# Kernel tuning notes

Hardware: AMD Instinct MI355X
Metric: run time of the kernel (lower is better)

Reference implementation:

```python
import jax, jax.numpy as jnp
import numpy as np

NL, D, DI, N, R, K = 32, 256, 512, 16, 16, 4   # layers, d_model, d_inner, d_state, dt_rank, d_conv
V, FF, BATCH, L = 4096, 1024, 32, 256


def _mamba_layer(x, p):
    # x: (B, L, D). One pre-norm Mamba block with residual: x + mamba(LN(x)).
    ln_w, ln_b, in_w, cw, cb, xp_w, dtw, dtb, A_log, Dskip, out_w = p
    mu = x.mean(-1, keepdims=True)
    var = ((x - mu) ** 2).mean(-1, keepdims=True)
    h = (x - mu) / jnp.sqrt(var + 1e-5) * ln_w + ln_b
    xz = jnp.einsum('bld,ed->ble', h, in_w)            # (B, L, 2*DI)
    xm, z = jnp.split(xz, 2, axis=-1)
    seq = xm.shape[1]
    # causal depthwise conv1d, kernel K, then SiLU
    xpad = jnp.pad(xm, ((0, 0), (K - 1, 0), (0, 0)))
    xc = sum(xpad[:, k:k + seq] * cw[:, k] for k in range(K)) + cb
    xc = jax.nn.silu(xc)
    dbc = jnp.einsum('ble,fe->blf', xc, xp_w)          # (B, L, R+2N)
    dt, Bm, Cm = jnp.split(dbc, [R, R + N], axis=-1)
    dt = jax.nn.softplus(jnp.einsum('blr,er->ble', dt, dtw) + dtb)  # (B, L, DI)
    A = -jnp.exp(A_log)                                # (DI, N)

    def step(hs, inp):
        dt_t, B_t, C_t, x_t = inp                      # (B,DI),(B,N),(B,N),(B,DI)
        dA = jnp.exp(dt_t[..., None] * A)              # (B, DI, N)
        hs = hs * dA + (dt_t * x_t)[..., None] * B_t[:, None, :]
        return hs, jnp.einsum('ben,bn->be', hs, C_t)

    h0 = jnp.zeros((xc.shape[0], DI, N), xc.dtype)
    _, ys = jax.lax.scan(step, h0, (dt.swapaxes(0, 1), Bm.swapaxes(0, 1), Cm.swapaxes(0, 1), xc.swapaxes(0, 1)))
    y = ys.swapaxes(0, 1) + xc * Dskip
    y = y * jax.nn.silu(z)
    return x + jnp.einsum('ble,de->bld', y, out_w)


def _stack_forward(x, params):
    return jax.lax.scan(lambda c, p: (jax.checkpoint(_mamba_layer)(c, p), None), x, params)[0]


def setup_inputs() -> dict:
    key = jax.random.key(0)
    ks = jax.random.split(key, 12)
    rn = lambda k, shape, s=0.02: jax.random.normal(k, shape, jnp.float32) * s
    return {
        'token_ids': jax.random.randint(ks[0], (BATCH, L), 0, V),
        'emb': rn(ks[1], (V, D)),
        'ln_w': jnp.ones((NL, D)), 'ln_b': jnp.zeros((NL, D)),
        'in_proj_w': rn(ks[2], (NL, 2 * DI, D)),
        'conv_w': rn(ks[3], (NL, DI, K), 0.1), 'conv_b': jnp.zeros((NL, DI)),
        'x_proj_w': rn(ks[4], (NL, R + 2 * N, DI)),
        'dt_w': rn(ks[5], (NL, DI, R), 0.1),
        'dt_b': jnp.full((NL, DI), float(np.log(np.expm1(0.01))), jnp.float32),
        'A_log': jnp.broadcast_to(jnp.log(jnp.arange(1, N + 1, dtype=jnp.float32)), (NL, DI, N)) + 0.0,
        'Dskip': jnp.ones((NL, DI)),
        'out_proj_w': rn(ks[6], (NL, D, DI)),
        'W1': rn(ks[7], (FF, D)), 'b1': jnp.zeros((FF,)),
        'W2': rn(ks[8], (V, FF)), 'b2': jnp.zeros((V,)),
    }


def reference(token_ids, emb, ln_w, ln_b, in_proj_w, conv_w, conv_b, x_proj_w, dt_w, dt_b, A_log, Dskip, out_proj_w, W1, b1, W2, b2):
    x = emb[token_ids]                                  # (B, L, D)
    params = (ln_w, ln_b, in_proj_w, conv_w, conv_b, x_proj_w, dt_w, dt_b, A_log, Dskip, out_proj_w)
    x = _stack_forward(x, params)                       # 32 stacked Mamba blocks
    h = jax.nn.relu(x @ W1.T + b1)
    return h @ W2.T + b2                                # (B, L, V) logits
```

## Files before the change

### kernel.cpp

```cpp
#include <hip/hip_runtime.h>
#include <hip/hip_bf16.h>
#include <cstdint>
#include <cstddef>


typedef __bf16 v8bf __attribute__((ext_vector_type(8)));
typedef float  v4f  __attribute__((ext_vector_type(4)));

__device__ __forceinline__ void async_copy16(const void* g, void* l) {
  __builtin_amdgcn_global_load_lds((const __attribute__((address_space(1))) void*)g,
                                   (__attribute__((address_space(3))) void*)l, 16, 0, 0);
}

__device__ __forceinline__ float bf(__bf16 v) { return (float)v; }

constexpr size_t OFF_WIN  = 0;
constexpr size_t OFF_WXP  = 16777216;
constexpr size_t OFF_WOUT = 18350080;
constexpr size_t OFF_WW1  = 26738688;
constexpr size_t OFF_WW2  = 27262976;
constexpr size_t OFF_X    = 35651584;
constexpr size_t OFF_H    = 44040192;
constexpr size_t OFF_XZ   = 48234496;
constexpr size_t OFF_DBC  = 65011712;
constexpr size_t OFF_PART = 66584576;
constexpr size_t OFF_SS   = 82313216;
constexpr size_t OFF_A2   = 83296256;

__global__ __launch_bounds__(256)
void f2b_multi(const float* __restrict__ s0, const float* __restrict__ s1,
               const float* __restrict__ s2, const float* __restrict__ s3,
               const float* __restrict__ s4, const float* __restrict__ s5,
               char* __restrict__ ws) {
  size_t i = (size_t)blockIdx.x * 256 + threadIdx.x;
  if (i < 8388608) { ((__bf16*)(ws + OFF_WIN))[i] = (__bf16)s0[i]; return; }
  i -= 8388608;
  if (i < 786432)  { ((__bf16*)(ws + OFF_WXP))[i] = (__bf16)s1[i]; return; }
  i -= 786432;
  if (i < 4194304) { ((__bf16*)(ws + OFF_WOUT))[i] = (__bf16)s2[i]; return; }
  i -= 4194304;
  if (i < 262144)  { ((__bf16*)(ws + OFF_WW1))[i] = (__bf16)s3[i]; return; }
  i -= 262144;
  if (i < 4194304) { ((__bf16*)(ws + OFF_WW2))[i] = (__bf16)s4[i]; return; }
  i -= 4194304;
  ((float*)(ws + OFF_A2))[i] = -1.4426950408889634f * __expf(s5[i]);
}

__global__ __launch_bounds__(256) void f2b_k(const float* __restrict__ X,
                                             __bf16* __restrict__ O) {
  size_t i = (size_t)blockIdx.x * 256 + threadIdx.x;
  O[i] = (__bf16)X[i];
}

__global__ __launch_bounds__(256)
void embed_ln_k(const int* __restrict__ tok, const float* __restrict__ emb,
                const float* __restrict__ w, const float* __restrict__ b,
                float* __restrict__ X, __bf16* __restrict__ H) {
  int row = blockIdx.x;
  int t   = threadIdx.x;
  float v = emb[(size_t)tok[row] * 256 + t];
  X[(size_t)row * 256 + t] = v;
  float s = v, q = v * v;
  #pragma unroll
  for (int o = 32; o > 0; o >>= 1) { s += __shfl_xor(s, o); q += __shfl_xor(q, o); }
  __shared__ float ss[4], qq[4];
  int wv = t >> 6;
  if ((t & 63) == 0) { ss[wv] = s; qq[wv] = q; }
  __syncthreads();
  s = ss[0] + ss[1] + ss[2] + ss[3];
  q = qq[0] + qq[1] + qq[2] + qq[3];
  float mu  = s * (1.f / 256.f);
  float var = q * (1.f / 256.f) - mu * mu;
  float r   = rsqrtf(var + 1e-5f);
  H[(size_t)row * 256 + t] = (__bf16)((v - mu) * r * w[t] + b[t]);
}

template <int EPI>
__global__ __launch_bounds__(256, 2)
void gemm_bt(const __bf16* __restrict__ A, const __bf16* __restrict__ W,
             void* outp, const float* __restrict__ bias, int M, int N, int K) {
  __shared__ __align__(16) __bf16 sA[128 * 32];
  __shared__ __align__(16) __bf16 sB[128 * 32];
  const int tid  = threadIdx.x;
  const int bm0  = blockIdx.y << 7;
  const int bn0  = blockIdx.x << 7;
  const int lane = tid & 63;
  const int wv   = tid >> 6;
  const int wm   = (wv >> 1) << 6;
  const int wn   = (wv & 1) << 6;
  const int lr   = lane & 15;
  const int lk   = lane >> 4;

  v4f acc[4][4] = {};

  const int r0 = tid >> 2;
  const int c0 = (tid & 3) << 3;
  const int wbase = (tid & ~63) << 3;

  const __bf16* gA0 = A + (size_t)(bm0 + r0) * K + c0;
  const __bf16* gA1 = A + (size_t)(bm0 + 64 + r0) * K + c0;
  const __bf16* gB0 = W + (size_t)(bn0 + r0) * K + c0;
  const __bf16* gB1 = W + (size_t)(bn0 + 64 + r0) * K + c0;

  for (int kk = 0; kk < K; kk += 32) {
    async_copy16(gA0 + kk, sA + wbase);
    async_copy16(gA1 + kk, sA + 2048 + wbase);
    async_copy16(gB0 + kk, sB + wbase);
    async_copy16(gB1 + kk, sB + 2048 + wbase);
    __syncthreads();
    v8bf af[4], bfr[4];
    #pragma unroll
    for (int i = 0; i < 4; ++i)
      af[i] = *(const v8bf*)(sA + ((wm + i * 16 + lr) << 5) + (lk << 3));
    #pragma unroll
    for (int j = 0; j < 4; ++j)
      bfr[j] = *(const v8bf*)(sB + ((wn + j * 16 + lr) << 5) + (lk << 3));
    #pragma unroll
    for (int i = 0; i < 4; ++i)
      #pragma unroll
      for (int j = 0; j < 4; ++j)
        acc[i][j] = __builtin_amdgcn_mfma_f32_16x16x32_bf16(af[i], bfr[j], acc[i][j], 0, 0, 0);
    __syncthreads();
  }

  #pragma unroll
  for (int i = 0; i < 4; ++i) {
    #pragma unroll
    for (int j = 0; j < 4; ++j) {
      int gc = bn0 + wn + j * 16 + lr;
      #pragma unroll
      for (int v = 0; v < 4; ++v) {
        int gr = bm0 + wm + i * 16 + (lk << 2) + v;
        float val = acc[i][j][v];
        size_t idx = (size_t)gr * N + gc;
        if (EPI == 0) {
          ((__bf16*)outp)[idx] = (__bf16)val;
        } else if (EPI == 1) {
          val += bias[gc]; val = fmaxf(val, 0.f);
          ((__bf16*)outp)[idx] = (__bf16)val;
        } else {
          ((float*)outp)[idx] = val + bias[gc];
        }
      }
    }
  }
}

__global__ __launch_bounds__(512, 4)
void convscan1_k(const __bf16* __restrict__ XZ,
                 const float* __restrict__ cw, const float* __restrict__ cb,
                 const __bf16* __restrict__ Wxp,
                 const float* __restrict__ dtw, const float* __restrict__ dtb,
                 const float* __restrict__ A2,
                 float* __restrict__ DBC,
                 float* __restrict__ PART, float* __restrict__ SS) {
  __shared__ __align__(16) __bf16 sXC[16 * 512];
  __shared__ __align__(16) float  sDBC[16 * 48];
  const int tid = threadIdx.x;
  const int c   = blockIdx.x >> 5;
  const int b   = blockIdx.x & 31;
  const int bl0 = b * 256 + c * 16;

  {
    const int r  = tid >> 5;
    const int ec = tid & 31;
    #pragma unroll
    for (int j = 0; j < 2; ++j) {
      const int e = (ec << 3) + (j << 8);
      v4f cw4[8];
      #pragma unroll
      for (int jj = 0; jj < 8; ++jj) cw4[jj] = *(const v4f*)(cw + (size_t)(e + jj) * 4);
      float a[8];
      #pragma unroll
      for (int jj = 0; jj < 8; ++jj) a[jj] = cb[e + jj];
      #pragma unroll
      for (int k = 0; k < 4; ++k) {
        if (c > 0 || r + k >= 3) {
          const v8bf xv = *(const v8bf*)(XZ + (size_t)(bl0 + r + k - 3) * 1024 + e);
          #pragma unroll
          for (int jj = 0; jj < 8; ++jj) a[jj] += bf(xv[jj]) * cw4[jj][k];
        }
      }
      v8bf outv;
      #pragma unroll
      for (int jj = 0; jj < 8; ++jj) {
        float s = a[jj] / (1.f + __expf(-a[jj]));
        outv[jj] = (__bf16)s;
      }
      const int cbk = (e >> 3) ^ (r & 7);
      *(v8bf*)(sXC + r * 512 + (cbk << 3)) = outv;
    }
  }
  __syncthreads();

  if (tid < 192) {
    const int w = tid >> 6, lane = tid & 63, lr = lane & 15, lk = lane >> 4;
    v4f acc = {};
    for (int kk = 0; kk < 512; kk += 32) {
      const v8bf bfr = *(const v8bf*)(Wxp + (size_t)(w * 16 + lr) * 512 + kk + (lk << 3));
      const int cbk = (((kk >> 3) + lk) ^ (lr & 7));
      const v8bf af = *(const v8bf*)(sXC + lr * 512 + (cbk << 3));
      acc = __builtin_amdgcn_mfma_f32_16x16x32_bf16(af, bfr, acc, 0, 0, 0);
    }
    const int gc = w * 16 + lr;
    #pragma unroll
    for (int v = 0; v < 4; ++v)
      sDBC[((lk << 2) + v) * 48 + gc] = acc[v];
  }
  __syncthreads();

  if (tid < 192)
    *(v4f*)(DBC + (size_t)bl0 * 48 + tid * 4) = *(const v4f*)(sDBC + tid * 4);

  if (c < 15) {
    const int e = tid;
    v4f a2[4], wd[4];
    #pragma unroll
    for (int q = 0; q < 4; ++q) {
      a2[q] = *(const v4f*)(A2  + (size_t)e * 16 + q * 4);
      wd[q] = *(const v4f*)(dtw + (size_t)e * 16 + q * 4);
    }
    const float bias = dtb[e];
    float part[16];
    #pragma unroll
    for (int n = 0; n < 16; ++n) part[n] = 0.f;
    float S = 0.f;
    for (int tt = 0; tt < 16; ++tt) {
      const v4f* dp = (const v4f*)(sDBC + tt * 48);
      float dtv = bias;
      {
        const v4f d0 = dp[0], d1 = dp[1], d2 = dp[2], d3 = dp[3];
        #pragma unroll
        for (int r = 0; r < 4; ++r)
          dtv += d0[r] * wd[0][r] + d1[r] * wd[1][r] + d2[r] * wd[2][r] + d3[r] * wd[3][r];
      }
      dtv = (dtv > 20.f) ? dtv : log1pf(__expf(dtv));
      const float x = bf(sXC[tt * 512 + (((e >> 3) ^ (tt & 7)) << 3) + (e & 7)]);
      const float dtx = dtv * x;
      S += dtv;
      {
        const v4f bv0 = dp[4], bv1 = dp[5], bv2 = dp[6], bv3 = dp[7];
        #pragma unroll
        for (int v = 0; v < 4; ++v) {
          part[v]      = part[v]      * exp2f(dtv * a2[0][v]) + dtx * bv0[v];
          part[4 + v]  = part[4 + v]  * exp2f(dtv * a2[1][v]) + dtx * bv1[v];
          part[8 + v]  = part[8 + v]  * exp2f(dtv * a2[2][v]) + dtx * bv2[v];
          part[12 + v] = part[12 + v] * exp2f(dtv * a2[3][v]) + dtx * bv3[v];
        }
      }
    }
    const size_t o = (((size_t)c * 32 + b) * 512 + e) * 16;
    #pragma unroll
    for (int rq = 0; rq < 4; ++rq) {
      v4f p;
      #pragma unroll
      for (int v = 0; v < 4; ++v) p[v] = part[rq * 4 + v];
      *(v4f*)(PART + o + rq * 4) = p;
    }
    SS[((size_t)c * 32 + b) * 512 + e] = S;
  }
}

__global__ __launch_bounds__(512, 4)
void scan2out_k(const __bf16* __restrict__ XZ,
                const float* __restrict__ cw, const float* __restrict__ cb,
                const float* __restrict__ DBC,
                const float* __restrict__ dtw, const float* __restrict__ dtb,
                const float* __restrict__ A2, const float* __restrict__ Dskip,
                const float* __restrict__ PART, const float* __restrict__ SS,
                const __bf16* __restrict__ Wout,
                const float* __restrict__ lnw, const float* __restrict__ lnb,
                float* __restrict__ X, __bf16* __restrict__ H) {
  __shared__ __align__(16) __bf16 sY[16 * 520];
  __shared__ __align__(16) __bf16 sB[256 * 32];
  __shared__ float sSum[8][16], sSq[8][16];
  const int tid = threadIdx.x;
  const int c   = blockIdx.x >> 5;
  const int b   = blockIdx.x & 31;
  const int bl0 = b * 256 + c * 16;
  const int e   = tid;

  v4f a2[4], wd[4];
  #pragma unroll
  for (int q = 0; q < 4; ++q) {
    a2[q] = *(const v4f*)(A2  + (size_t)e * 16 + q * 4);
    wd[q] = *(const v4f*)(dtw + (size_t)e * 16 + q * 4);
  }
  const float bias = dtb[e];
  const float Dsk  = Dskip[e];
  const v4f   cwv  = *(const v4f*)(cw + (size_t)e * 4);
  const float cbe  = cb[e];

  float h[16];
  #pragma unroll
  for (int n = 0; n < 16; ++n) h[n] = 0.f;
  for (int cc = 0; cc < c; ++cc) {
    const float S  = SS[((size_t)cc * 32 + b) * 512 + e];
    const size_t o = (((size_t)cc * 32 + b) * 512 + e) * 16;
    #pragma unroll
    for (int rq = 0; rq < 4; ++rq) {
      const v4f p = *(const v4f*)(PART + o + rq * 4);
      #pragma unroll
      for (int v = 0; v < 4; ++v)
        h[rq * 4 + v] = h[rq * 4 + v] * exp2f(a2[rq][v] * S) + p[v];
    }
  }

  float w0 = 0.f, w1 = 0.f, w2 = 0.f;
  if (c > 0) {
    w0 = bf(XZ[(size_t)(bl0 - 3) * 1024 + e]);
    w1 = bf(XZ[(size_t)(bl0 - 2) * 1024 + e]);
    w2 = bf(XZ[(size_t)(bl0 - 1) * 1024 + e]);
  }

  for (int tt = 0; tt < 16; ++tt) {
    const float xt = bf(XZ[(size_t)(bl0 + tt) * 1024 + e]);
    float a = cbe + w0 * cwv[0] + w1 * cwv[1] + w2 * cwv[2] + xt * cwv[3];
    const float x = a / (1.f + __expf(-a));
    w0 = w1; w1 = w2; w2 = xt;
    const v4f* dp = (const v4f*)(DBC + (size_t)(bl0 + tt) * 48);
    float dtv = bias;
    {
      const v4f d0 = dp[0], d1 = dp[1], d2 = dp[2], d3 = dp[3];
      #pragma unroll
      for (int r = 0; r < 4; ++r)
        dtv += d0[r] * wd[0][r] + d1[r] * wd[1][r] + d2[r] * wd[2][r] + d3[r] * wd[3][r];
    }
    dtv = (dtv > 20.f) ? dtv : log1pf(__expf(dtv));
    const float dtx = dtv * x;
    float y = 0.f;
    {
      const v4f bv0 = dp[4], bv1 = dp[5], bv2 = dp[6], bv3 = dp[7];
      const v4f cv0 = dp[8], cv1 = dp[9], cv2 = dp[10], cv3 = dp[11];
      #pragma unroll
      for (int v = 0; v < 4; ++v) {
        h[v]      = h[v]      * exp2f(dtv * a2[0][v]) + dtx * bv0[v];  y += h[v]      * cv0[v];
        h[4 + v]  = h[4 + v]  * exp2f(dtv * a2[1][v]) + dtx * bv1[v];  y += h[4 + v]  * cv1[v];
        h[8 + v]  = h[8 + v]  * exp2f(dtv * a2[2][v]) + dtx * bv2[v];  y += h[8 + v]  * cv2[v];
        h[12 + v] = h[12 + v] * exp2f(dtv * a2[3][v]) + dtx * bv3[v];  y += h[12 + v] * cv3[v];
      }
    }
    const float z  = bf(XZ[(size_t)(bl0 + tt) * 1024 + 512 + e]);
    const float sg = z / (1.f + __expf(-z));
    sY[tt * 520 + e] = (__bf16)((y + x * Dsk) * sg);
  }
  __syncthreads();

  const int w = tid >> 6, lane = tid & 63, lr = lane & 15, lk = lane >> 4;
  const int wn = w << 5;
  v4f acc[2] = {};
  for (int kk = 0; kk < 512; kk += 32) {
    async_copy16(Wout + (size_t)(tid >> 2) * 512 + ((tid & 3) << 3) + kk,
                 sB + ((tid & ~63) << 3));
    async_copy16(Wout + (size_t)(128 + (tid >> 2)) * 512 + ((tid & 3) << 3) + kk,
                 sB + 4096 + ((tid & ~63) << 3));
    __syncthreads();
    const v8bf af = *(const v8bf*)(sY + lr * 520 + kk + (lk << 3));
    #pragma unroll
    for (int j = 0; j < 2; ++j) {
      const v8bf bfr = *(const v8bf*)(sB + ((wn + j * 16 + lr) << 5) + (lk << 3));
      acc[j] = __builtin_amdgcn_mfma_f32_16x16x32_bf16(af, bfr, acc[j], 0, 0, 0);
    }
    __syncthreads();
  }

  float s2[4], q2[4];
  #pragma unroll
  for (int v = 0; v < 4; ++v) {
    const int gr = bl0 + (lk << 2) + v;
    float s = 0.f, q = 0.f;
    #pragma unroll
    for (int j = 0; j < 2; ++j) {
      const int gc = wn + j * 16 + lr;
      float val = X[(size_t)gr * 256 + gc] + acc[j][v];
      acc[j][v] = val;
      s += val; q += val * val;
    }
    #pragma unroll
    for (int o = 8; o > 0; o >>= 1) { s += __shfl_xor(s, o); q += __shfl_xor(q, o); }
    s2[v] = s; q2[v] = q;
  }
  if (lr == 0) {
    #pragma unroll
    for (int v = 0; v < 4; ++v) {
      const int row = (lk << 2) + v;
      sSum[w][row] = s2[v];
      sSq[w][row]  = q2[v];
    }
  }
  __syncthreads();
  #pragma unroll
  for (int v = 0; v < 4; ++v) {
    const int row = (lk << 2) + v;
    float S = 0.f, Q = 0.f;
    #pragma unroll
    for (int ww = 0; ww < 8; ++ww) { S += sSum[ww][row]; Q += sSq[ww][row]; }
    const float mu   = S * (1.f / 256.f);
    const float var  = Q * (1.f / 256.f) - mu * mu;
    const float rinv = rsqrtf(var + 1e-5f);
    const int gr = bl0 + row;
    #pragma unroll
    for (int j = 0; j < 2; ++j) {
      const int gc = wn + j * 16 + lr;
      const float val = acc[j][v];
      X[(size_t)gr * 256 + gc] = val;
      H[(size_t)gr * 256 + gc] = (__bf16)((val - mu) * rinv * lnw[gc] + lnb[gc]);
    }
  }
}

extern "C" void kernel_launch(void* const* d_in, const int* in_sizes, int n_in,
                              void* d_out, int out_size, void* d_ws, size_t ws_size,
                              hipStream_t stream) {
  const int*   tok  = (const int*)d_in[0];
  const float* emb  = (const float*)d_in[1];
  const float* lnw  = (const float*)d_in[2];
  const float* lnb  = (const float*)d_in[3];
  const float* inw  = (const float*)d_in[4];
  const float* cw   = (const float*)d_in[5];
  const float* cb   = (const float*)d_in[6];
  const float* xpw  = (const float*)d_in[7];
  const float* dtw  = (const float*)d_in[8];
  const float* dtb  = (const float*)d_in[9];
  const float* alog = (const float*)d_in[10];
  const float* dsk  = (const float*)d_in[11];
  const float* outw = (const float*)d_in[12];
  const float* W1   = (const float*)d_in[13];
  const float* b1   = (const float*)d_in[14];
  const float* W2   = (const float*)d_in[15];
  const float* b2   = (const float*)d_in[16];

  char* ws = (char*)d_ws;
  __bf16* WIN   = (__bf16*)(ws + OFF_WIN);
  __bf16* WXP   = (__bf16*)(ws + OFF_WXP);
  __bf16* WOUT  = (__bf16*)(ws + OFF_WOUT);
  __bf16* WW1   = (__bf16*)(ws + OFF_WW1);
  __bf16* WW2   = (__bf16*)(ws + OFF_WW2);
  float*  X     = (float*)(ws + OFF_X);
  __bf16* H     = (__bf16*)(ws + OFF_H);
  __bf16* XZ    = (__bf16*)(ws + OFF_XZ);
  float*  DBC   = (float*)(ws + OFF_DBC);
  float*  PART  = (float*)(ws + OFF_PART);
  float*  SS    = (float*)(ws + OFF_SS);
  float*  A2    = (float*)(ws + OFF_A2);
  __bf16* XB    = (__bf16*)(ws + OFF_PART);
  __bf16* HH    = (__bf16*)(ws + OFF_PART + 8388608);

  f2b_multi<<<70656, 256, 0, stream>>>(inw, xpw, outw, W1, W2, alog, ws);
  embed_ln_k<<<8192, 256, 0, stream>>>(tok, emb, lnw, lnb, X, H);

  for (int l = 0; l < 32; ++l) {
    const float*  cw_l   = cw   + (size_t)l * 512 * 4;
    const float*  cb_l   = cb   + (size_t)l * 512;
    const __bf16* xpw_l  = WXP  + (size_t)l * 48 * 512;
    const float*  dtw_l  = dtw  + (size_t)l * 512 * 16;
    const float*  dtb_l  = dtb  + (size_t)l * 512;
    const float*  A2_l   = A2   + (size_t)l * 512 * 16;
    const float*  dsk_l  = dsk  + (size_t)l * 512;
    const __bf16* inw_l  = WIN  + (size_t)l * 1024 * 256;
    const __bf16* outw_l = WOUT + (size_t)l * 256 * 512;
    const int lnx = (l + 1 < 32) ? l + 1 : 31;

    gemm_bt<0><<<dim3(8, 64), 256, 0, stream>>>(H, inw_l, XZ, nullptr, 8192, 1024, 256);
    convscan1_k<<<512, 512, 0, stream>>>(XZ, cw_l, cb_l, xpw_l, dtw_l, dtb_l,
                                         A2_l, DBC, PART, SS);
    scan2out_k<<<512, 512, 0, stream>>>(XZ, cw_l, cb_l, DBC, dtw_l, dtb_l,
                                        A2_l, dsk_l, PART, SS, outw_l,
                                        lnw + (size_t)lnx * 256,
                                        lnb + (size_t)lnx * 256, X, H);
  }

  f2b_k<<<8192, 256, 0, stream>>>(X, XB);
  gemm_bt<1><<<dim3(8, 64), 256, 0, stream>>>(XB, WW1, HH, b1, 8192, 1024, 256);
  gemm_bt<2><<<dim3(32, 64), 256, 0, stream>>>(HH, WW2, (float*)d_out, b2, 8192, 4096, 1024);
}
```

Baseline: 4.244 ms.

## Fuse in_proj GEMM into conv/scan kernels and widen chunks to 32 rows

Removes the standalone in_proj GEMM. The x-half is computed inside the conv kernel, recomputing 3 halo rows per chunk, and the z-half is computed inside the scan/out_proj kernel. Only the post-conv activations (XC) go to global memory, so the full XZ buffer is no longer written and re-read, and each layer drops one launch. The chunk length doubles from 16 to 32 rows, which halves the grid to 256 blocks of 512 threads and lengthens the serial scan per block. That trades occupancy and parallelism for less memory traffic.

```diff
diff --git a/kernel.cpp b/kernel.cpp
--- a/kernel.cpp
+++ b/kernel.cpp
@@ -21,7 +21,7 @@
 constexpr size_t OFF_WW2  = 27262976;
 constexpr size_t OFF_X    = 35651584;
 constexpr size_t OFF_H    = 44040192;
-constexpr size_t OFF_XZ   = 48234496;
+constexpr size_t OFF_XC   = 48234496;
 constexpr size_t OFF_DBC  = 65011712;
 constexpr size_t OFF_PART = 66584576;
 constexpr size_t OFF_SS   = 82313216;
@@ -146,27 +146,91 @@
   }
 }
 
-__global__ __launch_bounds__(512, 4)
-void convscan1_k(const __bf16* __restrict__ XZ,
+__global__ __launch_bounds__(512, 2)
+void k2_inconv_k(const __bf16* __restrict__ H, const __bf16* __restrict__ Wi,
                  const float* __restrict__ cw, const float* __restrict__ cb,
                  const __bf16* __restrict__ Wxp,
                  const float* __restrict__ dtw, const float* __restrict__ dtb,
                  const float* __restrict__ A2,
-                 float* __restrict__ DBC,
+                 __bf16* __restrict__ XC, float* __restrict__ DBC,
                  float* __restrict__ PART, float* __restrict__ SS) {
-  __shared__ __align__(16) __bf16 sXC[16 * 512];
-  __shared__ __align__(16) float  sDBC[16 * 48];
+  __shared__ __align__(16) char sm[93184];
+  __bf16* const sH   = (__bf16*)sm;
+  __bf16* const sB   = (__bf16*)(sm + 24576);
+  __bf16* const sXM  = (__bf16*)(sm + 57344);
+  __bf16* const sXC  = (__bf16*)(sm + 24576);
+  float*  const sDBC = (float*)sm;
+
   const int tid = threadIdx.x;
   const int c   = blockIdx.x >> 5;
   const int b   = blockIdx.x & 31;
-  const int bl0 = b * 256 + c * 16;
-
+  const int bl0 = b * 256 + c * 32;
+  const int lane = tid & 63, wv = tid >> 6;
+  const int lr = lane & 15, lk = lane >> 4;
+
+  #pragma unroll
+  for (int rnd = 0; rnd < 3; ++rnd) {
+    const int q = rnd * 512 + tid;
+    if (q < 1120) {
+      const int row = q >> 5, cc = q & 31;
+      int hr = bl0 - 3 + row; if (hr < 0) hr = 0;
+      const v8bf hv = *(const v8bf*)(H + (size_t)hr * 256 + (cc << 3));
+      *(v8bf*)(sH + row * 256 + ((cc ^ (row & 7)) << 3)) = hv;
+    }
+  }
+  __syncthreads();
+
+  const int wn = wv << 6;
   {
-    const int r  = tid >> 5;
-    const int ec = tid & 31;
-    #pragma unroll
-    for (int j = 0; j < 2; ++j) {
-      const int e = (ec << 3) + (j << 8);
+    v4f acc[3][4] = {};
+    for (int kk = 0; kk < 256; kk += 32) {
+      #pragma unroll
+      for (int rnd = 0; rnd < 4; ++rnd) {
+        const int q = rnd * 512 + tid;
+        const int n = q >> 2, cbs = (q & 3) ^ (n & 3);
+        async_copy16(Wi + (size_t)n * 256 + kk + (cbs << 3), sB + ((q & ~63) << 3));
+      }
+      __syncthreads();
+      v8bf af[3], bfr[4];
+      #pragma unroll
+      for (int i = 0; i < 3; ++i) {
+        const int row = i * 16 + lr;
+        af[i] = *(const v8bf*)(sH + row * 256 + ((((kk >> 3) + lk) ^ (row & 7)) << 3));
+      }
+      #pragma unroll
+      for (int j = 0; j < 4; ++j) {
+        const int n = wn + j * 16 + lr;
+        bfr[j] = *(const v8bf*)(sB + n * 32 + ((lk ^ (n & 3)) << 3));
+      }
+      #pragma unroll
+      for (int i = 0; i < 3; ++i)
+        #pragma unroll
+        for (int j = 0; j < 4; ++j)
+          acc[i][j] = __builtin_amdgcn_mfma_f32_16x16x32_bf16(af[i], bfr[j], acc[i][j], 0, 0, 0);
+      __syncthreads();
+    }
+    #pragma unroll
+    for (int i = 0; i < 3; ++i)
+      #pragma unroll
+      for (int v = 0; v < 4; ++v) {
+        const int row = i * 16 + (lk << 2) + v;
+        if (row < 35) {
+          #pragma unroll
+          for (int j = 0; j < 4; ++j) {
+            float val = acc[i][j][v];
+            if (c == 0 && row < 3) val = 0.f;
+            sXM[row * 512 + wn + j * 16 + lr] = (__bf16)val;
+          }
+        }
+      }
+  }
+  __syncthreads();
+
+  {
+    const int r = tid >> 4, ec = tid & 15;
+    #pragma unroll
+    for (int j = 0; j < 4; ++j) {
+      const int e = (ec << 3) + (j << 7);
       v4f cw4[8];
       #pragma unroll
       for (int jj = 0; jj < 8; ++jj) cw4[jj] = *(const v4f*)(cw + (size_t)(e + jj) * 4);
@@ -175,64 +239,69 @@
       for (int jj = 0; jj < 8; ++jj) a[jj] = cb[e + jj];
       #pragma unroll
       for (int k = 0; k < 4; ++k) {
-        if (c > 0 || r + k >= 3) {
-          const v8bf xv = *(const v8bf*)(XZ + (size_t)(bl0 + r + k - 3) * 1024 + e);
-          #pragma unroll
-          for (int jj = 0; jj < 8; ++jj) a[jj] += bf(xv[jj]) * cw4[jj][k];
-        }
+        const v8bf xv = *(const v8bf*)(sXM + (r + k) * 512 + e);
+        #pragma unroll
+        for (int jj = 0; jj < 8; ++jj) a[jj] += bf(xv[jj]) * cw4[jj][k];
       }
       v8bf outv;
       #pragma unroll
       for (int jj = 0; jj < 8; ++jj) {
-        float s = a[jj] / (1.f + __expf(-a[jj]));
+        const float s = a[jj] / (1.f + __expf(-a[jj]));
         outv[jj] = (__bf16)s;
       }
       const int cbk = (e >> 3) ^ (r & 7);
       *(v8bf*)(sXC + r * 512 + (cbk << 3)) = outv;
+      *(v8bf*)(XC + (size_t)(bl0 + r) * 512 + e) = outv;
     }
   }
   __syncthreads();
 
   if (tid < 192) {
-    const int w = tid >> 6, lane = tid & 63, lr = lane & 15, lk = lane >> 4;
-    v4f acc = {};
+    const int w = tid >> 6;
+    v4f accp[2] = {};
     for (int kk = 0; kk < 512; kk += 32) {
       const v8bf bfr = *(const v8bf*)(Wxp + (size_t)(w * 16 + lr) * 512 + kk + (lk << 3));
-      const int cbk = (((kk >> 3) + lk) ^ (lr & 7));
-      const v8bf af = *(const v8bf*)(sXC + lr * 512 + (cbk << 3));
-      acc = __builtin_amdgcn_mfma_f32_16x16x32_bf16(af, bfr, acc, 0, 0, 0);
+      #pragma unroll
+      for (int i = 0; i < 2; ++i) {
+        const int row = i * 16 + lr;
+        const int cbk = (((kk >> 3) + lk) ^ (row & 7));
+        const v8bf af = *(const v8bf*)(sXC + row * 512 + (cbk << 3));
+        accp[i] = __builtin_amdgcn_mfma_f32_16x16x32_bf16(af, bfr, accp[i], 0, 0, 0);
+      }
     }
     const int gc = w * 16 + lr;
     #pragma unroll
-    for (int v = 0; v < 4; ++v)
-      sDBC[((lk << 2) + v) * 48 + gc] = acc[v];
-  }
-  __syncthreads();
-
-  if (tid < 192)
+    for (int i = 0; i < 2; ++i)
+      #pragma unroll
+      for (int v = 0; v < 4; ++v)
+        sDBC[(i * 16 + (lk << 2) + v) * 48 + gc] = accp[i][v];
+  }
+  __syncthreads();
+
+  if (tid < 384)
     *(v4f*)(DBC + (size_t)bl0 * 48 + tid * 4) = *(const v4f*)(sDBC + tid * 4);
 
-  if (c < 15) {
+  if (c < 7) {
     const int e = tid;
-    v4f a2[4], wd[4];
+    v4f a2v[4], wd[4];
     #pragma unroll
     for (int q = 0; q < 4; ++q) {
-      a2[q] = *(const v4f*)(A2  + (size_t)e * 16 + q * 4);
-      wd[q] = *(const v4f*)(dtw + (size_t)e * 16 + q * 4);
+      a2v[q] = *(const v4f*)(A2  + (size_t)e * 16 + q * 4);
+      wd[q]  = *(const v4f*)(dtw + (size_t)e * 16 + q * 4);
     }
     const float bias = dtb[e];
     float part[16];
     #pragma unroll
     for (int n = 0; n < 16; ++n) part[n] = 0.f;
     float S = 0.f;
-    for (int tt = 0; tt < 16; ++tt) {
+    for (int tt = 0; tt < 32; ++tt) {
       const v4f* dp = (const v4f*)(sDBC + tt * 48);
       float dtv = bias;
       {
         const v4f d0 = dp[0], d1 = dp[1], d2 = dp[2], d3 = dp[3];
         #pragma unroll
-        for (int r = 0; r < 4; ++r)
-          dtv += d0[r] * wd[0][r] + d1[r] * wd[1][r] + d2[r] * wd[2][r] + d3[r] * wd[3][r];
+        for (int r2 = 0; r2 < 4; ++r2)
+          dtv += d0[r2] * wd[0][r2] + d1[r2] * wd[1][r2] + d2[r2] * wd[2][r2] + d3[r2] * wd[3][r2];
       }
       dtv = (dtv > 20.f) ? dtv : log1pf(__expf(dtv));
       const float x = bf(sXC[tt * 512 + (((e >> 3) ^ (tt & 7)) << 3) + (e & 7)]);
@@ -242,10 +311,10 @@
         const v4f bv0 = dp[4], bv1 = dp[5], bv2 = dp[6], bv3 = dp[7];
         #pragma unroll
         for (int v = 0; v < 4; ++v) {
-          part[v]      = part[v]      * exp2f(dtv * a2[0][v]) + dtx * bv0[v];
-          part[4 + v]  = part[4 + v]  * exp2f(dtv * a2[1][v]) + dtx * bv1[v];
-          part[8 + v]  = part[8 + v]  * exp2f(dtv * a2[2][v]) + dtx * bv2[v];
-          part[12 + v] = part[12 + v] * exp2f(dtv * a2[3][v]) + dtx * bv3[v];
+          part[v]      = part[v]      * exp2f(dtv * a2v[0][v]) + dtx * bv0[v];
+          part[4 + v]  = part[4 + v]  * exp2f(dtv * a2v[1][v]) + dtx * bv1[v];
+          part[8 + v]  = part[8 + v]  * exp2f(dtv * a2v[2][v]) + dtx * bv2[v];
+          part[12 + v] = part[12 + v] * exp2f(dtv * a2v[3][v]) + dtx * bv3[v];
         }
       }
     }
@@ -261,36 +330,90 @@
   }
 }
 
-__global__ __launch_bounds__(512, 4)
-void scan2out_k(const __bf16* __restrict__ XZ,
-                const float* __restrict__ cw, const float* __restrict__ cb,
-                const float* __restrict__ DBC,
+__global__ __launch_bounds__(512, 2)
+void k3_zscan_k(const __bf16* H, const __bf16* __restrict__ Wz,
+                const __bf16* __restrict__ XC, const float* __restrict__ DBC,
                 const float* __restrict__ dtw, const float* __restrict__ dtb,
                 const float* __restrict__ A2, const float* __restrict__ Dskip,
                 const float* __restrict__ PART, const float* __restrict__ SS,
                 const __bf16* __restrict__ Wout,
                 const float* __restrict__ lnw, const float* __restrict__ lnb,
-                float* __restrict__ X, __bf16* __restrict__ H) {
-  __shared__ __align__(16) __bf16 sY[16 * 520];
-  __shared__ __align__(16) __bf16 sB[256 * 32];
-  __shared__ float sSum[8][16], sSq[8][16];
+                float* __restrict__ X, __bf16* Hout) {
+  __shared__ __align__(16) char sm[83968];
+  __bf16* const sH   = (__bf16*)sm;
+  __bf16* const sBz  = (__bf16*)(sm + 16384);
+  __bf16* const sY   = (__bf16*)sm;
+  __bf16* const sB3  = (__bf16*)(sm + 33280);
+  float*  const sSum = (float*)(sm + 49664);
+  float*  const sSq  = (float*)(sm + 50176);
+  __bf16* const sZ   = (__bf16*)(sm + 50688);
+
   const int tid = threadIdx.x;
   const int c   = blockIdx.x >> 5;
   const int b   = blockIdx.x & 31;
-  const int bl0 = b * 256 + c * 16;
-  const int e   = tid;
-
-  v4f a2[4], wd[4];
+  const int bl0 = b * 256 + c * 32;
+  const int lane = tid & 63, wv = tid >> 6;
+  const int lr = lane & 15, lk = lane >> 4;
+
+  #pragma unroll
+  for (int rnd = 0; rnd < 2; ++rnd) {
+    const int q = rnd * 512 + tid;
+    const int row = q >> 5, cc = q & 31;
+    const v8bf hv = *(const v8bf*)(H + (size_t)(bl0 + row) * 256 + (cc << 3));
+    *(v8bf*)(sH + row * 256 + ((cc ^ (row & 7)) << 3)) = hv;
+  }
+  __syncthreads();
+
+  const int wn = wv << 6;
+  {
+    v4f acc[2][4] = {};
+    for (int kk = 0; kk < 256; kk += 32) {
+      #pragma unroll
+      for (int rnd = 0; rnd < 4; ++rnd) {
+        const int q = rnd * 512 + tid;
+        const int n = q >> 2, cbs = (q & 3) ^ (n & 3);
+        async_copy16(Wz + (size_t)n * 256 + kk + (cbs << 3), sBz + ((q & ~63) << 3));
+      }
+      __syncthreads();
+      v8bf af[2], bfr[4];
+      #pragma unroll
+      for (int i = 0; i < 2; ++i) {
+        const int row = i * 16 + lr;
+        af[i] = *(const v8bf*)(sH + row * 256 + ((((kk >> 3) + lk) ^ (row & 7)) << 3));
+      }
+      #pragma unroll
+      for (int j = 0; j < 4; ++j) {
+        const int n = wn + j * 16 + lr;
+        bfr[j] = *(const v8bf*)(sBz + n * 32 + ((lk ^ (n & 3)) << 3));
+      }
+      #pragma unroll
+      for (int i = 0; i < 2; ++i)
+        #pragma unroll
+        for (int j = 0; j < 4; ++j)
+          acc[i][j] = __builtin_amdgcn_mfma_f32_16x16x32_bf16(af[i], bfr[j], acc[i][j], 0, 0, 0);
+      __syncthreads();
+    }
+    #pragma unroll
+    for (int i = 0; i < 2; ++i)
+      #pragma unroll
+      for (int v = 0; v < 4; ++v) {
+        const int row = i * 16 + (lk << 2) + v;
+        #pragma unroll
+        for (int j = 0; j < 4; ++j)
+          sZ[row * 520 + wn + j * 16 + lr] = (__bf16)acc[i][j][v];
+      }
+  }
+  __syncthreads();
+
+  const int e = tid;
+  v4f a2v[4], wd[4];
   #pragma unroll
   for (int q = 0; q < 4; ++q) {
-    a2[q] = *(const v4f*)(A2  + (size_t)e * 16 + q * 4);
-    wd[q] = *(const v4f*)(dtw + (size_t)e * 16 + q * 4);
+    a2v[q] = *(const v4f*)(A2  + (size_t)e * 16 + q * 4);
+    wd[q]  = *(const v4f*)(dtw + (size_t)e * 16 + q * 4);
   }
   const float bias = dtb[e];
   const float Dsk  = Dskip[e];
-  const v4f   cwv  = *(const v4f*)(cw + (size_t)e * 4);
-  const float cbe  = cb[e];
-
   float h[16];
   #pragma unroll
   for (int n = 0; n < 16; ++n) h[n] = 0.f;
@@ -302,29 +425,19 @@
       const v4f p = *(const v4f*)(PART + o + rq * 4);
       #pragma unroll
       for (int v = 0; v < 4; ++v)
-        h[rq * 4 + v] = h[rq * 4 + v] * exp2f(a2[rq][v] * S) + p[v];
-    }
-  }
-
-  float w0 = 0.f, w1 = 0.f, w2 = 0.f;
-  if (c > 0) {
-    w0 = bf(XZ[(size_t)(bl0 - 3) * 1024 + e]);
-    w1 = bf(XZ[(size_t)(bl0 - 2) * 1024 + e]);
-    w2 = bf(XZ[(size_t)(bl0 - 1) * 1024 + e]);
-  }
-
-  for (int tt = 0; tt < 16; ++tt) {
-    const float xt = bf(XZ[(size_t)(bl0 + tt) * 1024 + e]);
-    float a = cbe + w0 * cwv[0] + w1 * cwv[1] + w2 * cwv[2] + xt * cwv[3];
-    const float x = a / (1.f + __expf(-a));
-    w0 = w1; w1 = w2; w2 = xt;
+        h[rq * 4 + v] = h[rq * 4 + v] * exp2f(a2v[rq][v] * S) + p[v];
+    }
+  }
+
+  for (int tt = 0; tt < 32; ++tt) {
+    const float x = bf(XC[(size_t)(bl0 + tt) * 512 + e]);
     const v4f* dp = (const v4f*)(DBC + (size_t)(bl0 + tt) * 48);
     float dtv = bias;
     {
       const v4f d0 = dp[0], d1 = dp[1], d2 = dp[2], d3 = dp[3];
       #pragma unroll
-      for (int r = 0; r < 4; ++r)
-        dtv += d0[r] * wd[0][r] + d1[r] * wd[1][r] + d2[r] * wd[2][r] + d3[r] * wd[3][r];
+      for (int r2 = 0; r2 < 4; ++r2)
+        dtv += d0[r2] * wd[0][r2] + d1[r2] * wd[1][r2] + d2[r2] * wd[2][r2] + d3[r2] * wd[3][r2];
     }
     dtv = (dtv > 20.f) ? dtv : log1pf(__expf(dtv));
     const float dtx = dtv * x;
@@ -334,32 +447,32 @@
       const v4f cv0 = dp[8], cv1 = dp[9], cv2 = dp[10], cv3 = dp[11];
       #pragma unroll
       for (int v = 0; v < 4; ++v) {
-        h[v]      = h[v]      * exp2f(dtv * a2[0][v]) + dtx * bv0[v];  y += h[v]      * cv0[v];
-        h[4 + v]  = h[4 + v]  * exp2f(dtv * a2[1][v]) + dtx * bv1[v];  y += h[4 + v]  * cv1[v];
-        h[8 + v]  = h[8 + v]  * exp2f(dtv * a2[2][v]) + dtx * bv2[v];  y += h[8 + v]  * cv2[v];
-        h[12 + v] = h[12 + v] * exp2f(dtv * a2[3][v]) + dtx * bv3[v];  y += h[12 + v] * cv3[v];
-      }
-    }
-    const float z  = bf(XZ[(size_t)(bl0 + tt) * 1024 + 512 + e]);
+        h[v]      = h[v]      * exp2f(dtv * a2v[0][v]) + dtx * bv0[v];  y += h[v]      * cv0[v];
+        h[4 + v]  = h[4 + v]  * exp2f(dtv * a2v[1][v]) + dtx * bv1[v];  y += h[4 + v]  * cv1[v];
+        h[8 + v]  = h[8 + v]  * exp2f(dtv * a2v[2][v]) + dtx * bv2[v];  y += h[8 + v]  * cv2[v];
+        h[12 + v] = h[12 + v] * exp2f(dtv * a2v[3][v]) + dtx * bv3[v];  y += h[12 + v] * cv3[v];
+      }
+    }
+    const float z  = bf(sZ[tt * 520 + e]);
     const float sg = z / (1.f + __expf(-z));
     sY[tt * 520 + e] = (__bf16)((y + x * Dsk) * sg);
   }
   __syncthreads();
 
-  const int w = tid >> 6, lane = tid & 63, lr = lane & 15, lk = lane >> 4;
-  const int wn = w << 5;
-  v4f acc[2] = {};
+  const int wm = (wv & 1) << 4;
+  const int wn3 = (wv >> 1) << 6;
+  v4f acc3[4] = {};
   for (int kk = 0; kk < 512; kk += 32) {
     async_copy16(Wout + (size_t)(tid >> 2) * 512 + ((tid & 3) << 3) + kk,
-                 sB + ((tid & ~63) << 3));
+                 sB3 + ((tid & ~63) << 3));
     async_copy16(Wout + (size_t)(128 + (tid >> 2)) * 512 + ((tid & 3) << 3) + kk,
-                 sB + 4096 + ((tid & ~63) << 3));
+                 sB3 + 4096 + ((tid & ~63) << 3));
     __syncthreads();
-    const v8bf af = *(const v8bf*)(sY + lr * 520 + kk + (lk << 3));
-    #pragma unroll
-    for (int j = 0; j < 2; ++j) {
-      const v8bf bfr = *(const v8bf*)(sB + ((wn + j * 16 + lr) << 5) + (lk << 3));
-      acc[j] = __builtin_amdgcn_mfma_f32_16x16x32_bf16(af, bfr, acc[j], 0, 0, 0);
+    const v8bf af = *(const v8bf*)(sY + (wm + lr) * 520 + kk + (lk << 3));
+    #pragma unroll
+    for (int j = 0; j < 4; ++j) {
+      const v8bf bfr = *(const v8bf*)(sB3 + ((wn3 + j * 16 + lr) << 5) + (lk << 3));
+      acc3[j] = __builtin_amdgcn_mfma_f32_16x16x32_bf16(af, bfr, acc3[j], 0, 0, 0);
     }
     __syncthreads();
   }
@@ -367,13 +480,13 @@
   float s2[4], q2[4];
   #pragma unroll
   for (int v = 0; v < 4; ++v) {
-    const int gr = bl0 + (lk << 2) + v;
+    const int gr = bl0 + wm + (lk << 2) + v;
     float s = 0.f, q = 0.f;
     #pragma unroll
-    for (int j = 0; j < 2; ++j) {
-      const int gc = wn + j * 16 + lr;
-      float val = X[(size_t)gr * 256 + gc] + acc[j][v];
-      acc[j][v] = val;
+    for (int j = 0; j < 4; ++j) {
+      const int gc = wn3 + j * 16 + lr;
+      float val = X[(size_t)gr * 256 + gc] + acc3[j][v];
+      acc3[j][v] = val;
       s += val; q += val * val;
     }
     #pragma unroll
@@ -383,28 +496,27 @@
   if (lr == 0) {
     #pragma unroll
     for (int v = 0; v < 4; ++v) {
-      const int row = (lk << 2) + v;
-      sSum[w][row] = s2[v];
-      sSq[w][row]  = q2[v];
+      const int row = wm + (lk << 2) + v;
+      sSum[(wv >> 1) * 32 + row] = s2[v];
+      sSq[(wv >> 1) * 32 + row]  = q2[v];
     }
   }
   __syncthreads();
   #pragma unroll
   for (int v = 0; v < 4; ++v) {
-    const int row = (lk << 2) + v;
-    float S = 0.f, Q = 0.f;
-    #pragma unroll
-    for (int ww = 0; ww < 8; ++ww) { S += sSum[ww][row]; Q += sSq[ww][row]; }
+    const int row = wm + (lk << 2) + v;
+    const float S = sSum[row] + sSum[32 + row] + sSum[64 + row] + sSum[96 + row];
+    const float Q = sSq[row]  + sSq[32 + row]  + sSq[64 + row]  + sSq[96 + row];
     const float mu   = S * (1.f / 256.f);
     const float var  = Q * (1.f / 256.f) - mu * mu;
     const float rinv = rsqrtf(var + 1e-5f);
     const int gr = bl0 + row;
     #pragma unroll
-    for (int j = 0; j < 2; ++j) {
-      const int gc = wn + j * 16 + lr;
-      const float val = acc[j][v];
+    for (int j = 0; j < 4; ++j) {
+      const int gc = wn3 + j * 16 + lr;
+      const float val = acc3[j][v];
       X[(size_t)gr * 256 + gc] = val;
-      H[(size_t)gr * 256 + gc] = (__bf16)((val - mu) * rinv * lnw[gc] + lnb[gc]);
+      Hout[(size_t)gr * 256 + gc] = (__bf16)((val - mu) * rinv * lnw[gc] + lnb[gc]);
     }
   }
 }
@@ -438,7 +550,7 @@
   __bf16* WW2   = (__bf16*)(ws + OFF_WW2);
   float*  X     = (float*)(ws + OFF_X);
   __bf16* H     = (__bf16*)(ws + OFF_H);
-  __bf16* XZ    = (__bf16*)(ws + OFF_XZ);
+  __bf16* XC    = (__bf16*)(ws + OFF_XC);
   float*  DBC   = (float*)(ws + OFF_DBC);
   float*  PART  = (float*)(ws + OFF_PART);
   float*  SS    = (float*)(ws + OFF_SS);
@@ -450,22 +562,22 @@
   embed_ln_k<<<8192, 256, 0, stream>>>(tok, emb, lnw, lnb, X, H);
 
   for (int l = 0; l < 32; ++l) {
-    const float*  cw_l   = cw   + (size_t)l * 512 * 4;
+    const __bf16* Wi_l   = WIN  + (size_t)l * 262144;
+    const __bf16* Wz_l   = WIN  + (size_t)l * 262144 + 131072;
+    const float*  cw_l   = cw   + (size_t)l * 2048;
     const float*  cb_l   = cb   + (size_t)l * 512;
-    const __bf16* xpw_l  = WXP  + (size_t)l * 48 * 512;
-    const float*  dtw_l  = dtw  + (size_t)l * 512 * 16;
+    const __bf16* xpw_l  = WXP  + (size_t)l * 24576;
+    const float*  dtw_l  = dtw  + (size_t)l * 8192;
     const float*  dtb_l  = dtb  + (size_t)l * 512;
-    const float*  A2_l   = A2   + (size_t)l * 512 * 16;
+    const float*  A2_l   = A2   + (size_t)l * 8192;
     const float*  dsk_l  = dsk  + (size_t)l * 512;
-    const __bf16* inw_l  = WIN  + (size_t)l * 1024 * 256;
-    const __bf16* outw_l = WOUT + (size_t)l * 256 * 512;
+    const __bf16* outw_l = WOUT + (size_t)l * 131072;
     const int lnx = (l + 1 < 32) ? l + 1 : 31;
 
-    gemm_bt<0><<<dim3(8, 64), 256, 0, stream>>>(H, inw_l, XZ, nullptr, 8192, 1024, 256);
-    convscan1_k<<<512, 512, 0, stream>>>(XZ, cw_l, cb_l, xpw_l, dtw_l, dtb_l,
-                                         A2_l, DBC, PART, SS);
-    scan2out_k<<<512, 512, 0, stream>>>(XZ, cw_l, cb_l, DBC, dtw_l, dtb_l,
-                                        A2_l, dsk_l, PART, SS, outw_l,
+    k2_inconv_k<<<256, 512, 0, stream>>>(H, Wi_l, cw_l, cb_l, xpw_l, dtw_l, dtb_l,
+                                         A2_l, XC, DBC, PART, SS);
+    k3_zscan_k<<<256, 512, 0, stream>>>(H, Wz_l, XC, DBC, dtw_l, dtb_l, A2_l,
+                                        dsk_l, PART, SS, outw_l,
                                         lnw + (size_t)lnx * 256,
                                         lnb + (size_t)lnx * 256, X, H);
   }
```

After: 4.126 ms. -2.8%, faster.
